# Performance work log

Hardware: AMD Instinct MI355X
Metric: run time of the kernel (lower is better)

## Reference

```python
import jax, jax.numpy as jnp
import numpy as np

EPS = 1e-8
LN_EPS = 1e-5
B, T, VDIM, ADIM, DM = 8, 2048, 1024, 768, 256
HID = 1024  # max(64, min(4*256, 2048))
DELTA_LOW, DELTA_HIGH = 2.0, 6.0
WINDOW = 5.0
GATE_MIN, GATE_MAX = 0.05, 0.95


def layer_norm(x):
    mu = jnp.mean(x, axis=-1, keepdims=True)
    var = jnp.var(x, axis=-1, keepdims=True)
    return (x - mu) / jnp.sqrt(var + LN_EPS)


def l2_normalize(x):
    n = jnp.sqrt(jnp.sum(x * x, axis=-1, keepdims=True))
    return x / jnp.maximum(n, EPS)


def setup_inputs() -> dict:
    key = jax.random.key(0)
    ks = jax.random.split(key, 8)
    inp = {
        "video_seq": jax.random.normal(ks[0], (B, T, VDIM), jnp.float32),
        "audio_seq": jax.random.normal(ks[1], (B, T, ADIM), jnp.float32),
        "Wv": jax.random.normal(ks[2], (VDIM, DM), jnp.float32) * (1.0 / np.sqrt(VDIM)),
        "bv": jnp.zeros((DM,), jnp.float32),
        "Wa": jax.random.normal(ks[3], (ADIM, DM), jnp.float32) * (1.0 / np.sqrt(ADIM)),
        "ba": jnp.zeros((DM,), jnp.float32),
        "theta": jnp.float32(0.0),
        "W1": jax.random.normal(ks[4], (3 * DM, HID), jnp.float32) * (1.0 / np.sqrt(3 * DM)),
        "b1": jnp.zeros((HID,), jnp.float32),
        "W2": jax.random.normal(ks[5], (HID, 1), jnp.float32) * (1.0 / np.sqrt(HID)),
        "b2": jnp.zeros((1,), jnp.float32),
    }
    return inp


def reference(video_seq, audio_seq, Wv, bv, Wa, ba, theta, W1, b1, W2, b2):
    v = layer_norm(video_seq @ Wv + bv)          # [B,T,DM]
    a = layer_norm(audio_seq @ Wa + ba)          # [B,T,DM]
    b, t, d = v.shape

    # LearnableDelay
    th = jnp.clip(theta, -12.0, 12.0)
    delta = DELTA_LOW + (DELTA_HIGH - DELTA_LOW) * jax.nn.sigmoid(th)
    delta_b = jnp.full((b,), delta, jnp.float32)

    # SoftTemporalShift (right shift with linear interpolation)
    dl = jnp.clip(delta_b, 0.0, float(t - 1))[:, None, None]   # [B,1,1]
    n = jnp.floor(dl)
    alpha = dl - n
    n_i = n.astype(jnp.int32)
    tidx = jnp.arange(t, dtype=jnp.int32)[None, :, None]       # [1,T,1]
    idx0 = jnp.clip(tidx - n_i, 0, t - 1)                      # [B,T,1]
    idx1 = jnp.clip(idx0 + 1, 0, t - 1)
    a0 = jnp.take_along_axis(a, jnp.broadcast_to(idx0, (b, t, d)), axis=1)
    a1 = jnp.take_along_axis(a, jnp.broadcast_to(idx1, (b, t, d)), axis=1)
    a_shift = (1.0 - alpha) * a0 + alpha * a1

    # DisplacementAwareCausalMask (hard, single scale)
    tf = jnp.arange(t, dtype=jnp.float32)
    tt = tf[None, :, None]                                     # t  -> [1,T,1]
    tau = tf[None, None, :]                                    # tau -> [1,1,T]
    center = jnp.minimum(jnp.maximum(tt + delta_b[:, None, None], 0.0), tt)
    raw = (jnp.abs(tau - center) <= WINDOW).astype(jnp.float32)
    raw = raw * (tau <= tt).astype(jnp.float32)
    M = raw / jnp.maximum(jnp.sum(raw, axis=-1, keepdims=True), EPS)  # [B,T,T]

    # mask-weighted audio context
    a_ctx = jnp.einsum('btk,bkd->btd', M, a_shift)

    # AlignmentGate (dropout inactive at eval)
    vn = l2_normalize(v)
    an = l2_normalize(a_ctx)
    x = jnp.concatenate([an, vn, an * vn], axis=-1)            # [B,T,3*DM]
    h = jax.nn.gelu(x @ W1 + b1, approximate=False)
    logits = jnp.clip(h @ W2 + b2, -12.0, 12.0)                # [B,T,1]
    g = jnp.clip(jax.nn.sigmoid(logits), GATE_MIN, GATE_MAX)

    fused = g * a_ctx + (1.0 - g) * v                          # [B,T,DM]
    return fused
```

## Files before the change

### kernel.cpp

```cpp
#include <hip/hip_runtime.h>
#include <cstdint>
#include <cstddef>

typedef unsigned short u16;
typedef unsigned int u32;
typedef __attribute__((ext_vector_type(8))) short short8;
typedef __attribute__((ext_vector_type(4))) float f32x4;

#define T_SEQ 2048
#define BT_ROWS 16384

__device__ __forceinline__ u16 f2bf(float x) {
  union { float f; u32 u; } v; v.f = x;
  u32 r = v.u + 0x7fffu + ((v.u >> 16) & 1u);
  return (u16)(r >> 16);
}
__device__ __forceinline__ u32 pkbf(float lo, float hi) {
  union { float f; u32 u; } a, b; a.f = lo; b.f = hi;
  const u32 ra = a.u + 0x7fffu + ((a.u >> 16) & 1u);
  const u32 rb = b.u + 0x7fffu + ((b.u >> 16) & 1u);
  return __builtin_amdgcn_perm(rb, ra, 0x07060302);
}
__device__ __forceinline__ float wave_bcast_sum(float x) {
#pragma unroll
  for (int off = 32; off > 0; off >>= 1) x += __shfl_down(x, off);
  return __shfl(x, 0);
}
__device__ __forceinline__ void gl_lds16(const void* g, void* l) {
  __builtin_amdgcn_global_load_lds((const __attribute__((address_space(1))) u32*)g,
                                   (__attribute__((address_space(3))) u32*)l, 16, 0, 0);
}
__device__ __forceinline__ float gelu_f(float x) {
  float z = 1.5957691216057308f * x * (1.0f + 0.044715f * x * x);
  float e = __expf(z);
  return x - x * __builtin_amdgcn_rcpf(1.0f + e);
}
__device__ __forceinline__ void lgkm_barrier() {
  asm volatile("s_waitcnt lgkmcnt(0)" ::: "memory");
  __builtin_amdgcn_s_barrier();
}

__global__ __launch_bounds__(256) void tcvt_all(const float* __restrict__ Wv,
                                                const float* __restrict__ Wa,
                                                const float* __restrict__ W1,
                                                u16* __restrict__ wvT,
                                                u16* __restrict__ waT,
                                                u16* __restrict__ w1T,
                                                float* __restrict__ logits) {
  int b = blockIdx.x;
  if (b >= 1216) {
    logits[(b - 1216) * 256 + threadIdx.x] = 0.0f;
    return;
  }
  __shared__ float tile[32][33];
  const float* in; u16* out; int K, N, bx, by;
  if (b < 256)      { in = Wv; out = wvT; K = 1024; N = 256;  bx = b & 31;  by = b >> 5; }
  else if (b < 448) { b -= 256; in = Wa; out = waT; K = 768; N = 256;  bx = b % 24; by = b / 24; }
  else              { b -= 448; in = W1; out = w1T; K = 768; N = 1024; bx = b % 24; by = b / 24; }
  const int k0 = bx * 32, n0 = by * 32;
  const int tx = threadIdx.x & 31, ty = threadIdx.x >> 5;
#pragma unroll
  for (int r = 0; r < 4; r++)
    tile[ty + r * 8][tx] = in[(size_t)(k0 + ty + r * 8) * N + n0 + tx];
  __syncthreads();
#pragma unroll
  for (int r = 0; r < 4; r++)
    out[(size_t)(n0 + ty + r * 8) * K + k0 + tx] = f2bf(tile[tx][ty + r * 8]);
}

template <int K>
__device__ __forceinline__ void proj_body(const float* __restrict__ A,
                                          const u16* __restrict__ Bt,
                                          const float* __restrict__ bias,
                                          float* __restrict__ C,
                                          int m0, u16* As, int k0) {
  constexpr int NT = K / 64;
  const int tid = threadIdx.x;
  const int wave = tid >> 6, lane = tid & 63, qm = lane & 15, quad = lane >> 4;
  const int cw = wave * 64;

  const int ar = tid >> 2;
  const float* Arow = A + (size_t)(m0 + ar) * K + (tid & 3) * 4;
  int awAddr[4];
#pragma unroll
  for (int g = 0; g < 4; g++) {
    const int cg = ((tid & 3) >> 1) + 2 * g;
    awAddr[g] = ar * 64 + ((cg ^ (ar & 7)) * 8) + (tid & 1) * 4;
  }
  const u16* brow[4];
#pragma unroll
  for (int j = 0; j < 4; j++)
    brow[j] = Bt + (size_t)(cw + j * 16 + qm) * K + quad * 8;

  f32x4 acc[4][4] = {};
  short8 bfrag[2][8];
  float4 p[4];

  int koff = k0;

#pragma unroll
  for (int g = 0; g < 4; g++) p[g] = *(const float4*)(Arow + koff + g * 16);
#pragma unroll
  for (int s = 0; s < 2; s++)
#pragma unroll
    for (int j = 0; j < 4; j++)
      bfrag[0][s * 4 + j] = *(const short8*)(brow[j] + koff + s * 32);
#pragma unroll
  for (int g = 0; g < 4; g++) {
    uint2 w; w.x = pkbf(p[g].x, p[g].y); w.y = pkbf(p[g].z, p[g].w);
    *(uint2*)&As[awAddr[g]] = w;
  }
  lgkm_barrier();

#pragma unroll
  for (int t = 0; t < NT; t++) {
    const int cb = t & 1, nb = cb ^ 1;
    int knext = koff + 64;
    if (knext == K) knext = 0;
    if (t + 1 < NT) {
#pragma unroll
      for (int g = 0; g < 4; g++)
        p[g] = *(const float4*)(Arow + knext + g * 16);
#pragma unroll
      for (int s = 0; s < 2; s++)
#pragma unroll
        for (int j = 0; j < 4; j++)
          bfrag[nb][s * 4 + j] = *(const short8*)(brow[j] + knext + s * 32);
    }
#pragma unroll
    for (int s = 0; s < 2; s++) {
      short8 af[4];
#pragma unroll
      for (int i = 0; i < 4; i++) {
        const int r = i * 16 + qm;
        af[i] = *(const short8*)&As[cb * 4096 + r * 64 + ((s * 4 + quad) ^ (r & 7)) * 8];
      }
      __builtin_amdgcn_s_setprio(1);
#pragma unroll
      for (int i = 0; i < 4; i++)
#pragma unroll
        for (int j = 0; j < 4; j++)
          acc[i][j] = __builtin_amdgcn_mfma_f32_16x16x32_bf16(
              af[i], bfrag[cb][s * 4 + j], acc[i][j], 0, 0, 0);
      __builtin_amdgcn_s_setprio(0);
    }
    if (t + 1 < NT) {
#pragma unroll
      for (int g = 0; g < 4; g++) {
        uint2 w; w.x = pkbf(p[g].x, p[g].y); w.y = pkbf(p[g].z, p[g].w);
        *(uint2*)&As[nb * 4096 + awAddr[g]] = w;
      }
      lgkm_barrier();
    }
    koff = knext;
  }

  float bcol[4];
#pragma unroll
  for (int j = 0; j < 4; j++) bcol[j] = bias[cw + j * 16 + qm];
#pragma unroll
  for (int i = 0; i < 4; i++)
#pragma unroll
    for (int j = 0; j < 4; j++)
#pragma unroll
      for (int r = 0; r < 4; r++)
        acc[i][j][r] += bcol[j];
  float s1[4][4], s2[4][4];
#pragma unroll
  for (int i = 0; i < 4; i++)
#pragma unroll
    for (int r = 0; r < 4; r++) {
      float a1 = 0, a2 = 0;
#pragma unroll
      for (int j = 0; j < 4; j++) { a1 += acc[i][j][r]; a2 += acc[i][j][r] * acc[i][j][r]; }
#pragma unroll
      for (int off = 1; off < 16; off <<= 1) {
        a1 += __shfl_xor(a1, off);
        a2 += __shfl_xor(a2, off);
      }
      s1[i][r] = a1; s2[i][r] = a2;
    }
  __syncthreads();
  float* red = (float*)As;
  if (qm == 0) {
#pragma unroll
    for (int i = 0; i < 4; i++)
#pragma unroll
      for (int r = 0; r < 4; r++) {
        const int row = i * 16 + quad * 4 + r;
        red[row * 8 + wave * 2] = s1[i][r];
        red[row * 8 + wave * 2 + 1] = s2[i][r];
      }
  }
  __syncthreads();
#pragma unroll
  for (int i = 0; i < 4; i++)
#pragma unroll
    for (int r = 0; r < 4; r++) {
      const int row = i * 16 + quad * 4 + r;
      const float4 q1 = *(const float4*)&red[row * 8];
      const float4 q2 = *(const float4*)&red[row * 8 + 4];
      const float st = q1.x + q1.z + q2.x + q2.z;
      const float st2 = q1.y + q1.w + q2.y + q2.w;
      const float mu = st * (1.0f / 256.0f);
      const float var = st2 * (1.0f / 256.0f) - mu * mu;
      const float inv = rsqrtf(var + 1e-5f);
#pragma unroll
      for (int j = 0; j < 4; j++)
        C[(size_t)(m0 + row) * 256 + cw + j * 16 + qm] = (acc[i][j][r] - mu) * inv;
    }
}

__global__ __launch_bounds__(256, 2) void proj_ln(const float* __restrict__ Vin,
                                                  const float* __restrict__ Ain,
                                                  const u16* __restrict__ wvT,
                                                  const u16* __restrict__ waT,
                                                  const float* __restrict__ bv,
                                                  const float* __restrict__ ba,
                                                  float* __restrict__ vOut,
                                                  float* __restrict__ aOut) {
  __shared__ __align__(16) u16 As[2][64 * 64];
  int b = blockIdx.x;
  if (b < 256)
    proj_body<1024>(Vin, wvT, bv, vOut, b * 64, &As[0][0], (b & 15) * 64);
  else {
    b -= 256;
    proj_body<768>(Ain, waT, ba, aOut, b * 64, &As[0][0], (b % 12) * 64);
  }
}

__global__ __launch_bounds__(256, 3) void gemm_gelu_w2(const u16* __restrict__ Axb,
                                                       const u16* __restrict__ Bt,
                                                       const float* __restrict__ b1,
                                                       const float* __restrict__ W2,
                                                       float* __restrict__ logits) {
  constexpr int K = 768;
  __shared__ u16 As[128 * 64];
  __shared__ u16 Bs[128 * 64];
  const int tid = threadIdx.x;
  const int n0 = blockIdx.x * 128;
  const int m0 = blockIdx.y * 128;
  const int wave = tid >> 6, lane = tid & 63, qm = lane & 15, quad = lane >> 4;
  const int rw = (wave >> 1) * 64, cw = (wave & 1) * 64;

  const int crow = tid >> 3;
  const int cpart = (tid & 7) ^ (crow & 7);
  const u16* Ap[4];
  const u16* Bp[4];
#pragma unroll
  for (int g = 0; g < 4; g++) {
    Ap[g] = Axb + (size_t)(m0 + crow + g * 32) * K + cpart * 8;
    Bp[g] = Bt + (size_t)(n0 + crow + g * 32) * K + cpart * 8;
  }

  f32x4 acc[4][4] = {};
  for (int kt = 0; kt < K; kt += 64) {
#pragma unroll
    for (int g = 0; g < 4; g++) gl_lds16(Ap[g] + kt, &As[(tid + g * 256) * 8]);
#pragma unroll
    for (int g = 0; g < 4; g++) gl_lds16(Bp[g] + kt, &Bs[(tid + g * 256) * 8]);
    __syncthreads();
#pragma unroll
    for (int s = 0; s < 2; s++) {
      short8 af[4], bfr[4];
#pragma unroll
      for (int i = 0; i < 4; i++) {
        const int r = rw + i * 16 + qm;
        af[i] = *(const short8*)&As[r * 64 + ((s * 4 + quad) ^ (r & 7)) * 8];
      }
#pragma unroll
      for (int j = 0; j < 4; j++) {
        const int r = cw + j * 16 + qm;
        bfr[j] = *(const short8*)&Bs[r * 64 + ((s * 4 + quad) ^ (r & 7)) * 8];
      }
#pragma unroll
      for (int i = 0; i < 4; i++)
#pragma unroll
        for (int j = 0; j < 4; j++)
          acc[i][j] = __builtin_amdgcn_mfma_f32_16x16x32_bf16(af[i], bfr[j], acc[i][j], 0, 0, 0);
    }
    __syncthreads();
  }

  float w2j[4], bc[4];
#pragma unroll
  for (int j = 0; j < 4; j++) {
    const int col = n0 + cw + j * 16 + qm;
    w2j[j] = W2[col];
    bc[j] = b1[col];
  }
#pragma unroll
  for (int i = 0; i < 4; i++) {
#pragma unroll
    for (int r = 0; r < 4; r++) {
      float p = 0.0f;
#pragma unroll
      for (int j = 0; j < 4; j++)
        p += gelu_f(acc[i][j][r] + bc[j]) * w2j[j];
      p += __shfl_xor(p, 1);
      p += __shfl_xor(p, 2);
      p += __shfl_xor(p, 4);
      p += __shfl_xor(p, 8);
      if (qm == 0)
        atomicAdd(&logits[m0 + rw + i * 16 + quad * 4 + r], p);
    }
  }
}

__global__ __launch_bounds__(256) void shift_norm(const float* __restrict__ a,
                                                  const float* __restrict__ v,
                                                  float* __restrict__ actx,
                                                  u16* __restrict__ xb,
                                                  const float* __restrict__ theta) {
  const int row = blockIdx.x * 4 + (threadIdx.x >> 6);
  const int lane = threadIdx.x & 63;
  const int d4 = lane * 4;
  const int bb = row >> 11;
  const int t = row & (T_SEQ - 1);
  const float th = fminf(fmaxf(theta[0], -12.0f), 12.0f);
  const float delta = 2.0f + 4.0f * (1.0f / (1.0f + expf(-th)));
  const float dl = fminf(fmaxf(delta, 0.0f), (float)(T_SEQ - 1));
  const float nf = floorf(dl);
  const float alpha = dl - nf;
  const int ni = (int)nf;
  const float center = fminf(fmaxf((float)t + delta, 0.0f), (float)t);
  float sx = 0, sy = 0, sz = 0, sw = 0, cnt = 0.0f;
  const float* ab = a + (size_t)bb * T_SEQ * 256;
#pragma unroll
  for (int j = 0; j < 6; j++) {
    const int tau = t - 5 + j;
    if (tau < 0) continue;
    if (fabsf((float)tau - center) > 5.0f) continue;
    cnt += 1.0f;
    const int i0 = min(max(tau - ni, 0), T_SEQ - 1);
    const int i1 = min(i0 + 1, T_SEQ - 1);
    const float4 a0 = *(const float4*)&ab[(size_t)i0 * 256 + d4];
    const float4 a1 = *(const float4*)&ab[(size_t)i1 * 256 + d4];
    sx += a0.x + alpha * (a1.x - a0.x);
    sy += a0.y + alpha * (a1.y - a0.y);
    sz += a0.z + alpha * (a1.z - a0.z);
    sw += a0.w + alpha * (a1.w - a0.w);
  }
  const float sc = 1.0f / fmaxf(cnt, 1e-8f);
  float4 o; o.x = sx * sc; o.y = sy * sc; o.z = sz * sc; o.w = sw * sc;
  *(float4*)&actx[(size_t)row * 256 + d4] = o;
  const float4 vv = *(const float4*)&v[(size_t)row * 256 + d4];
  float sa2 = o.x * o.x + o.y * o.y + o.z * o.z + o.w * o.w;
  float sv2 = vv.x * vv.x + vv.y * vv.y + vv.z * vv.z + vv.w * vv.w;
  sa2 = wave_bcast_sum(sa2);
  sv2 = wave_bcast_sum(sv2);
  const float ia = 1.0f / fmaxf(sqrtf(sa2), 1e-8f);
  const float iv = 1.0f / fmaxf(sqrtf(sv2), 1e-8f);
  const float anx = o.x * ia, any_ = o.y * ia, anz = o.z * ia, anw = o.w * ia;
  const float vnx = vv.x * iv, vny = vv.y * iv, vnz = vv.z * iv, vnw = vv.w * iv;
  u16* xr = xb + (size_t)row * 768;
  u32 pa[2] = {pkbf(anx, any_), pkbf(anz, anw)};
  u32 pv[2] = {pkbf(vnx, vny), pkbf(vnz, vnw)};
  u32 pp[2] = {pkbf(anx * vnx, any_ * vny), pkbf(anz * vnz, anw * vnw)};
  *(uint2*)&xr[d4] = *(uint2*)pa;
  *(uint2*)&xr[256 + d4] = *(uint2*)pv;
  *(uint2*)&xr[512 + d4] = *(uint2*)pp;
}

__global__ __launch_bounds__(256) void gate_mix(const float* __restrict__ logits,
                                                const float* __restrict__ b2,
                                                const float* __restrict__ actx,
                                                const float* __restrict__ v,
                                                float* __restrict__ out) {
  const int row = blockIdx.x * 4 + (threadIdx.x >> 6);
  const int lane = threadIdx.x & 63;
  const float l = fminf(fmaxf(logits[row] + b2[0], -12.0f), 12.0f);
  float g = 1.0f / (1.0f + expf(-l));
  g = fminf(fmaxf(g, 0.05f), 0.95f);
  const float4 aa = *(const float4*)&actx[(size_t)row * 256 + lane * 4];
  const float4 vv = *(const float4*)&v[(size_t)row * 256 + lane * 4];
  float4 o;
  o.x = g * aa.x + (1.0f - g) * vv.x;
  o.y = g * aa.y + (1.0f - g) * vv.y;
  o.z = g * aa.z + (1.0f - g) * vv.z;
  o.w = g * aa.w + (1.0f - g) * vv.w;
  *(float4*)&out[(size_t)row * 256 + lane * 4] = o;
}

extern "C" void kernel_launch(void* const* d_in, const int* in_sizes, int n_in,
                              void* d_out, int out_size, void* d_ws, size_t ws_size,
                              hipStream_t stream) {
  const float* video = (const float*)d_in[0];
  const float* audio = (const float*)d_in[1];
  const float* Wv    = (const float*)d_in[2];
  const float* bv    = (const float*)d_in[3];
  const float* Wa    = (const float*)d_in[4];
  const float* ba    = (const float*)d_in[5];
  const float* theta = (const float*)d_in[6];
  const float* W1    = (const float*)d_in[7];
  const float* b1    = (const float*)d_in[8];
  const float* W2    = (const float*)d_in[9];
  const float* b2    = (const float*)d_in[10];
  float* out = (float*)d_out;
  char* ws = (char*)d_ws;

  const size_t OFF_WVT = 0;
  const size_t OFF_WAT = 524288;
  const size_t OFF_W1T = 917504;
  const size_t OFF_LOG = 2490368;
  const size_t OFF_V   = 2555904;
  const size_t OFF_A   = 19333120;
  const size_t OFF_ACTX= 36110336;
  const size_t OFF_XB  = 52887552;

  u16* wvT = (u16*)(ws + OFF_WVT);
  u16* waT = (u16*)(ws + OFF_WAT);
  u16* w1T = (u16*)(ws + OFF_W1T);
  float* logits = (float*)(ws + OFF_LOG);
  float* v    = (float*)(ws + OFF_V);
  float* a    = (float*)(ws + OFF_A);
  float* actx = (float*)(ws + OFF_ACTX);
  u16* xb = (u16*)(ws + OFF_XB);

  tcvt_all<<<1280, 256, 0, stream>>>(Wv, Wa, W1, wvT, waT, w1T, logits);
  proj_ln<<<512, 256, 0, stream>>>(video, audio, wvT, waT, bv, ba, v, a);
  shift_norm<<<BT_ROWS / 4, 256, 0, stream>>>(a, v, actx, xb, theta);
  gemm_gelu_w2<<<dim3(8, BT_ROWS / 128), 256, 0, stream>>>(xb, w1T, b1, W2, logits);
  gate_mix<<<BT_ROWS / 4, 256, 0, stream>>>(logits, b2, actx, v, out);
}
```

Measured before the change: 240.5 us.

## Process 8 rows per wave in shift_norm with sliding-window reuse of audio loads

```diff
diff --git a/kernel.cpp b/kernel.cpp
--- a/kernel.cpp
+++ b/kernel.cpp
@@ -312,54 +312,95 @@
                                                   float* __restrict__ actx,
                                                   u16* __restrict__ xb,
                                                   const float* __restrict__ theta) {
-  const int row = blockIdx.x * 4 + (threadIdx.x >> 6);
-  const int lane = threadIdx.x & 63;
+  const int wave = threadIdx.x >> 6, lane = threadIdx.x & 63;
+  const int wrow = blockIdx.x * 32 + wave * 8;
   const int d4 = lane * 4;
-  const int bb = row >> 11;
-  const int t = row & (T_SEQ - 1);
+  const int bb = wrow >> 11;
+  const int tb = wrow & (T_SEQ - 1);
   const float th = fminf(fmaxf(theta[0], -12.0f), 12.0f);
   const float delta = 2.0f + 4.0f * (1.0f / (1.0f + expf(-th)));
   const float dl = fminf(fmaxf(delta, 0.0f), (float)(T_SEQ - 1));
   const float nf = floorf(dl);
   const float alpha = dl - nf;
   const int ni = (int)nf;
-  const float center = fminf(fmaxf((float)t + delta, 0.0f), (float)t);
-  float sx = 0, sy = 0, sz = 0, sw = 0, cnt = 0.0f;
   const float* ab = a + (size_t)bb * T_SEQ * 256;
-#pragma unroll
-  for (int j = 0; j < 6; j++) {
-    const int tau = t - 5 + j;
-    if (tau < 0) continue;
-    if (fabsf((float)tau - center) > 5.0f) continue;
-    cnt += 1.0f;
-    const int i0 = min(max(tau - ni, 0), T_SEQ - 1);
-    const int i1 = min(i0 + 1, T_SEQ - 1);
-    const float4 a0 = *(const float4*)&ab[(size_t)i0 * 256 + d4];
-    const float4 a1 = *(const float4*)&ab[(size_t)i1 * 256 + d4];
-    sx += a0.x + alpha * (a1.x - a0.x);
-    sy += a0.y + alpha * (a1.y - a0.y);
-    sz += a0.z + alpha * (a1.z - a0.z);
-    sw += a0.w + alpha * (a1.w - a0.w);
-  }
-  const float sc = 1.0f / fmaxf(cnt, 1e-8f);
-  float4 o; o.x = sx * sc; o.y = sy * sc; o.z = sz * sc; o.w = sw * sc;
-  *(float4*)&actx[(size_t)row * 256 + d4] = o;
-  const float4 vv = *(const float4*)&v[(size_t)row * 256 + d4];
-  float sa2 = o.x * o.x + o.y * o.y + o.z * o.z + o.w * o.w;
-  float sv2 = vv.x * vv.x + vv.y * vv.y + vv.z * vv.z + vv.w * vv.w;
-  sa2 = wave_bcast_sum(sa2);
-  sv2 = wave_bcast_sum(sv2);
-  const float ia = 1.0f / fmaxf(sqrtf(sa2), 1e-8f);
-  const float iv = 1.0f / fmaxf(sqrtf(sv2), 1e-8f);
-  const float anx = o.x * ia, any_ = o.y * ia, anz = o.z * ia, anw = o.w * ia;
-  const float vnx = vv.x * iv, vny = vv.y * iv, vnz = vv.z * iv, vnw = vv.w * iv;
-  u16* xr = xb + (size_t)row * 768;
-  u32 pa[2] = {pkbf(anx, any_), pkbf(anz, anw)};
-  u32 pv[2] = {pkbf(vnx, vny), pkbf(vnz, vnw)};
-  u32 pp[2] = {pkbf(anx * vnx, any_ * vny), pkbf(anz * vnz, anw * vnw)};
-  *(uint2*)&xr[d4] = *(uint2*)pa;
-  *(uint2*)&xr[256 + d4] = *(uint2*)pv;
-  *(uint2*)&xr[512 + d4] = *(uint2*)pp;
+
+  float4 o[8];
+  if (tb >= 16) {
+    const int s0 = tb - ni - 5;
+    const float* arow0 = ab + (size_t)s0 * 256 + d4;
+    float4 sum[8];
+#pragma unroll
+    for (int r = 0; r < 8; r++) { sum[r].x = 0; sum[r].y = 0; sum[r].z = 0; sum[r].w = 0; }
+    float4 prev = *(const float4*)(arow0);
+#pragma unroll
+    for (int m = 0; m < 13; m++) {
+      const float4 cur = *(const float4*)(arow0 + (size_t)(m + 1) * 256);
+      float4 g;
+      g.x = prev.x + alpha * (cur.x - prev.x);
+      g.y = prev.y + alpha * (cur.y - prev.y);
+      g.z = prev.z + alpha * (cur.z - prev.z);
+      g.w = prev.w + alpha * (cur.w - prev.w);
+#pragma unroll
+      for (int r = 0; r < 8; r++)
+        if (r <= m && m <= r + 5) {
+          sum[r].x += g.x; sum[r].y += g.y; sum[r].z += g.z; sum[r].w += g.w;
+        }
+      prev = cur;
+    }
+    const float sc = 1.0f / 6.0f;
+#pragma unroll
+    for (int r = 0; r < 8; r++) {
+      o[r].x = sum[r].x * sc; o[r].y = sum[r].y * sc;
+      o[r].z = sum[r].z * sc; o[r].w = sum[r].w * sc;
+    }
+  } else {
+#pragma unroll
+    for (int r = 0; r < 8; r++) {
+      const int t = tb + r;
+      const float center = fminf(fmaxf((float)t + delta, 0.0f), (float)t);
+      float sx = 0, sy = 0, sz = 0, sw = 0, cnt = 0.0f;
+#pragma unroll
+      for (int j = 0; j < 6; j++) {
+        const int tau = t - 5 + j;
+        if (tau < 0) continue;
+        if (fabsf((float)tau - center) > 5.0f) continue;
+        cnt += 1.0f;
+        const int i0 = min(max(tau - ni, 0), T_SEQ - 1);
+        const int i1 = min(i0 + 1, T_SEQ - 1);
+        const float4 a0 = *(const float4*)&ab[(size_t)i0 * 256 + d4];
+        const float4 a1 = *(const float4*)&ab[(size_t)i1 * 256 + d4];
+        sx += a0.x + alpha * (a1.x - a0.x);
+        sy += a0.y + alpha * (a1.y - a0.y);
+        sz += a0.z + alpha * (a1.z - a0.z);
+        sw += a0.w + alpha * (a1.w - a0.w);
+      }
+      const float sc = 1.0f / fmaxf(cnt, 1e-8f);
+      o[r].x = sx * sc; o[r].y = sy * sc; o[r].z = sz * sc; o[r].w = sw * sc;
+    }
+  }
+
+#pragma unroll
+  for (int r = 0; r < 8; r++) {
+    const int row = wrow + r;
+    *(float4*)&actx[(size_t)row * 256 + d4] = o[r];
+    const float4 vv = *(const float4*)&v[(size_t)row * 256 + d4];
+    float sa2 = o[r].x * o[r].x + o[r].y * o[r].y + o[r].z * o[r].z + o[r].w * o[r].w;
+    float sv2 = vv.x * vv.x + vv.y * vv.y + vv.z * vv.z + vv.w * vv.w;
+    sa2 = wave_bcast_sum(sa2);
+    sv2 = wave_bcast_sum(sv2);
+    const float ia = 1.0f / fmaxf(sqrtf(sa2), 1e-8f);
+    const float iv = 1.0f / fmaxf(sqrtf(sv2), 1e-8f);
+    const float anx = o[r].x * ia, any_ = o[r].y * ia, anz = o[r].z * ia, anw = o[r].w * ia;
+    const float vnx = vv.x * iv, vny = vv.y * iv, vnz = vv.z * iv, vnw = vv.w * iv;
+    u16* xr = xb + (size_t)row * 768;
+    u32 pa[2] = {pkbf(anx, any_), pkbf(anz, anw)};
+    u32 pv[2] = {pkbf(vnx, vny), pkbf(vnz, vnw)};
+    u32 pp[2] = {pkbf(anx * vnx, any_ * vny), pkbf(anz * vnz, anw * vnw)};
+    *(uint2*)&xr[d4] = *(uint2*)pa;
+    *(uint2*)&xr[256 + d4] = *(uint2*)pv;
+    *(uint2*)&xr[512 + d4] = *(uint2*)pp;
+  }
 }
 
 __global__ __launch_bounds__(256) void gate_mix(const float* __restrict__ logits,
@@ -419,7 +460,7 @@
 
   tcvt_all<<<1280, 256, 0, stream>>>(Wv, Wa, W1, wvT, waT, w1T, logits);
   proj_ln<<<512, 256, 0, stream>>>(video, audio, wvT, waT, bv, ba, v, a);
-  shift_norm<<<BT_ROWS / 4, 256, 0, stream>>>(a, v, actx, xb, theta);
+  shift_norm<<<BT_ROWS / 32, 256, 0, stream>>>(a, v, actx, xb, theta);
   gemm_gelu_w2<<<dim3(8, BT_ROWS / 128), 256, 0, stream>>>(xb, w1T, b1, W2, logits);
   gate_mix<<<BT_ROWS / 4, 256, 0, stream>>>(logits, b2, actx, v, out);
 }
```

Result: slower. 249.2 us (+3.6%).

## Restructure W1 GEMM: 128x256 tiles, double-buffered LDS, B fragments loaded direct to registers

Applied to the files above, without the earlier changes.

```diff
diff --git a/kernel.cpp b/kernel.cpp
--- a/kernel.cpp
+++ b/kernel.cpp
@@ -229,57 +229,87 @@
   }
 }
 
-__global__ __launch_bounds__(256, 3) void gemm_gelu_w2(const u16* __restrict__ Axb,
+__global__ __launch_bounds__(256, 2) void gemm_gelu_w2(const u16* __restrict__ Axb,
                                                        const u16* __restrict__ Bt,
                                                        const float* __restrict__ b1,
                                                        const float* __restrict__ W2,
                                                        float* __restrict__ logits) {
   constexpr int K = 768;
-  __shared__ u16 As[128 * 64];
-  __shared__ u16 Bs[128 * 64];
+  constexpr int NT = K / 64;
+  __shared__ __align__(16) u16 As[2][128 * 64];
   const int tid = threadIdx.x;
-  const int n0 = blockIdx.x * 128;
+  const int n0 = blockIdx.x * 256;
   const int m0 = blockIdx.y * 128;
   const int wave = tid >> 6, lane = tid & 63, qm = lane & 15, quad = lane >> 4;
-  const int rw = (wave >> 1) * 64, cw = (wave & 1) * 64;
-
-  const int crow = tid >> 3;
-  const int cpart = (tid & 7) ^ (crow & 7);
-  const u16* Ap[4];
-  const u16* Bp[4];
-#pragma unroll
-  for (int g = 0; g < 4; g++) {
-    Ap[g] = Axb + (size_t)(m0 + crow + g * 32) * K + cpart * 8;
-    Bp[g] = Bt + (size_t)(n0 + crow + g * 32) * K + cpart * 8;
-  }
-
-  f32x4 acc[4][4] = {};
-  for (int kt = 0; kt < K; kt += 64) {
-#pragma unroll
-    for (int g = 0; g < 4; g++) gl_lds16(Ap[g] + kt, &As[(tid + g * 256) * 8]);
-#pragma unroll
-    for (int g = 0; g < 4; g++) gl_lds16(Bp[g] + kt, &Bs[(tid + g * 256) * 8]);
-    __syncthreads();
+  const int cw = wave * 64;
+
+  const int ar = tid >> 1;
+  const u16* Arow = Axb + (size_t)(m0 + ar) * K + (tid & 1) * 32;
+  int awAddr[4];
+#pragma unroll
+  for (int c = 0; c < 4; c++) {
+    const int cg = (tid & 1) * 4 + c;
+    awAddr[c] = ar * 64 + ((cg ^ (ar & 7)) * 8);
+  }
+  const u16* brow[4];
+#pragma unroll
+  for (int j = 0; j < 4; j++)
+    brow[j] = Bt + (size_t)(n0 + cw + j * 16 + qm) * K + quad * 8;
+
+  f32x4 acc[8][4] = {};
+  short8 bfrag[2][8];
+  uint4 p[4];
+
+  int koff = (blockIdx.y % NT) * 64;
+
+#pragma unroll
+  for (int c = 0; c < 4; c++) p[c] = *(const uint4*)(Arow + koff + c * 8);
+#pragma unroll
+  for (int s = 0; s < 2; s++)
+#pragma unroll
+    for (int j = 0; j < 4; j++)
+      bfrag[0][s * 4 + j] = *(const short8*)(brow[j] + koff + s * 32);
+#pragma unroll
+  for (int c = 0; c < 4; c++) *(uint4*)&As[0][awAddr[c]] = p[c];
+  lgkm_barrier();
+
+#pragma unroll
+  for (int t = 0; t < NT; t++) {
+    const int cb = t & 1, nb = cb ^ 1;
+    int knext = koff + 64;
+    if (knext == K) knext = 0;
+    if (t + 1 < NT) {
+#pragma unroll
+      for (int c = 0; c < 4; c++) p[c] = *(const uint4*)(Arow + knext + c * 8);
+#pragma unroll
+      for (int s = 0; s < 2; s++)
+#pragma unroll
+        for (int j = 0; j < 4; j++)
+          bfrag[nb][s * 4 + j] = *(const short8*)(brow[j] + knext + s * 32);
+    }
 #pragma unroll
     for (int s = 0; s < 2; s++) {
-      short8 af[4], bfr[4];
-#pragma unroll
-      for (int i = 0; i < 4; i++) {
-        const int r = rw + i * 16 + qm;
-        af[i] = *(const short8*)&As[r * 64 + ((s * 4 + quad) ^ (r & 7)) * 8];
+      short8 af[8];
+#pragma unroll
+      for (int i = 0; i < 8; i++) {
+        const int r = i * 16 + qm;
+        af[i] = *(const short8*)&As[cb][r * 64 + ((s * 4 + quad) ^ (r & 7)) * 8];
       }
-#pragma unroll
-      for (int j = 0; j < 4; j++) {
-        const int r = cw + j * 16 + qm;
-        bfr[j] = *(const short8*)&Bs[r * 64 + ((s * 4 + quad) ^ (r & 7)) * 8];
-      }
-#pragma unroll
-      for (int i = 0; i < 4; i++)
+      __builtin_amdgcn_s_setprio(1);
+#pragma unroll
+      for (int i = 0; i < 8; i++)
 #pragma unroll
         for (int j = 0; j < 4; j++)
-          acc[i][j] = __builtin_amdgcn_mfma_f32_16x16x32_bf16(af[i], bfr[j], acc[i][j], 0, 0, 0);
-    }
-    __syncthreads();
+          acc[i][j] = __builtin_amdgcn_mfma_f32_16x16x32_bf16(
+              af[i], bfrag[cb][s * 4 + j], acc[i][j], 0, 0, 0);
+      __builtin_amdgcn_s_setprio(0);
+    }
+    if (t + 1 < NT) {
+#pragma unroll
+      for (int c = 0; c < 4; c++) *(uint4*)&As[nb][awAddr[c]] = p[c];
+      lgkm_barrier();
+    }
+    koff = knext;
   }
 
   float w2j[4], bc[4];
@@ -290,19 +320,19 @@
     bc[j] = b1[col];
   }
 #pragma unroll
-  for (int i = 0; i < 4; i++) {
+  for (int i = 0; i < 8; i++) {
 #pragma unroll
     for (int r = 0; r < 4; r++) {
-      float p = 0.0f;
+      float pl = 0.0f;
 #pragma unroll
       for (int j = 0; j < 4; j++)
-        p += gelu_f(acc[i][j][r] + bc[j]) * w2j[j];
-      p += __shfl_xor(p, 1);
-      p += __shfl_xor(p, 2);
-      p += __shfl_xor(p, 4);
-      p += __shfl_xor(p, 8);
+        pl += gelu_f(acc[i][j][r] + bc[j]) * w2j[j];
+      pl += __shfl_xor(pl, 1);
+      pl += __shfl_xor(pl, 2);
+      pl += __shfl_xor(pl, 4);
+      pl += __shfl_xor(pl, 8);
       if (qm == 0)
-        atomicAdd(&logits[m0 + rw + i * 16 + quad * 4 + r], p);
+        atomicAdd(&logits[m0 + i * 16 + quad * 4 + r], pl);
     }
   }
 }
@@ -420,6 +450,6 @@
   tcvt_all<<<1280, 256, 0, stream>>>(Wv, Wa, W1, wvT, waT, w1T, logits);
   proj_ln<<<512, 256, 0, stream>>>(video, audio, wvT, waT, bv, ba, v, a);
   shift_norm<<<BT_ROWS / 4, 256, 0, stream>>>(a, v, actx, xb, theta);
-  gemm_gelu_w2<<<dim3(8, BT_ROWS / 128), 256, 0, stream>>>(xb, w1T, b1, W2, logits);
+  gemm_gelu_w2<<<dim3(4, BT_ROWS / 128), 256, 0, stream>>>(xb, w1T, b1, W2, logits);
   gate_mix<<<BT_ROWS / 4, 256, 0, stream>>>(logits, b2, actx, v, out);
 }
```

New measurement: 262.2 us. 1.09x slower.
